# Kernel tuning notes

Hardware: AMD Instinct MI355X
Metric: run time of the kernel (lower is better)

The kernel has to match this reference:

```python
import jax, jax.numpy as jnp
import numpy as np

N = 50000   # nodes
E = 200000  # edges
C = 32      # conv_dim
ND = 75     # n_atom_features
ED = 12     # n_bond_features
L = 3       # num_layer
G = 500     # num graphs in batch
HID = 5     # neurons_message
EPS = 1e-5


def leaky(v):
    return jnp.where(v > 0, v, 0.01 * v)


def setup_inputs() -> dict:
    key = jax.random.key(0)
    ks = jax.random.split(key, 16)
    x = jax.random.normal(ks[0], (N, ND), jnp.float32)
    edge_index = jax.random.randint(ks[1], (2, E), 0, N, jnp.int32)
    edge_attr = jax.random.uniform(ks[2], (E, ED), jnp.float32)
    batch = jnp.sort(jax.random.randint(ks[3], (N,), 0, G, jnp.int32))
    return {
        "x": x,
        "edge_index": edge_index,
        "edge_attr": edge_attr,
        "batch": batch,
        "lin_W": jax.random.normal(ks[4], (ND, C), jnp.float32) * 0.1,
        "lin_b": jnp.zeros((C,), jnp.float32),
        "mes_W1": jax.random.normal(ks[5], (L, ED, HID), jnp.float32) * 0.3,
        "mes_b1": jnp.zeros((L, HID), jnp.float32),
        "mes_W2": jax.random.normal(ks[6], (L, HID, C * C), jnp.float32) * 0.05,
        "mes_b2": jnp.zeros((L, C * C), jnp.float32),
        "root_W": jax.random.normal(ks[7], (L, C, C), jnp.float32) * 0.1,
        "conv_b": jnp.zeros((L, C), jnp.float32),
        "bn_g": jnp.ones((L, C), jnp.float32),
        "bn_b": jnp.zeros((L, C), jnp.float32),
        "pred_W": jax.random.normal(ks[8], (C, 1), jnp.float32) * 0.1,
        "pred_b": jnp.zeros((1,), jnp.float32),
    }


def reference(x, edge_index, edge_attr, batch, lin_W, lin_b, mes_W1, mes_b1,
              mes_W2, mes_b2, root_W, conv_b, bn_g, bn_b, pred_W, pred_b):
    src, dst = edge_index[0], edge_index[1]
    # initial atom projection
    h = leaky(x @ lin_W + lin_b)  # [N, C]
    for l in range(L):
        # edge MLP -> per-edge weight matrix [E, C, C]
        w = jnp.maximum(edge_attr @ mes_W1[l] + mes_b1[l], 0.0)
        w = (w @ mes_W2[l] + mes_b2[l]).reshape(E, C, C)
        # gather source features, per-edge matmul, scatter-add to targets
        msg = jnp.einsum('ec,ecd->ed', h[src], w)  # [E, C]
        agg = jax.ops.segment_sum(msg, dst, num_segments=N)  # [N, C]
        out = agg + h @ root_W[l] + conv_b[l]
        # batch norm (batch statistics over nodes)
        mu = out.mean(axis=0)
        var = out.var(axis=0)
        out = (out - mu) / jnp.sqrt(var + EPS) * bn_g[l] + bn_b[l]
        if l < L - 1:
            out = leaky(out)
        h = out  # JK == 'last'
    # graph readout: scatter_add over batch ids, then prediction head
    g = jax.ops.segment_sum(h, batch, num_segments=G)  # [G, C]
    return g @ pred_W + pred_b  # [G, 1]
```

## Files before the change

### kernel.cpp

```cpp
#include <hip/hip_runtime.h>

namespace {

constexpr int kN = 50000, kE = 200000, kG = 500;
constexpr float kEps = 1e-5f;
constexpr int kNB = (kN + 255) / 256;
constexpr int kEB = (kE + 255) / 256;

typedef short v8s __attribute__((ext_vector_type(8)));
typedef float v4f __attribute__((ext_vector_type(4)));

__device__ __forceinline__ unsigned short bf16rn(float x) {
    unsigned u = __float_as_uint(x);
    return (unsigned short)((u + 0x7FFFu + ((u >> 16) & 1u)) >> 16);
}
__device__ __forceinline__ float bf16lo(unsigned p) { return __uint_as_float(p << 16); }
__device__ __forceinline__ float bf16hi(unsigned p) { return __uint_as_float(p & 0xFFFF0000u); }
__device__ __forceinline__ unsigned pk2(float a, float b) {
    return (unsigned)bf16rn(a) | ((unsigned)bf16rn(b) << 16);
}

__global__ __launch_bounds__(256) void zero_init(int* __restrict__ deg,
                                                 float* __restrict__ stats) {
    int i = blockIdx.x * 256 + threadIdx.x;
    if (i < kN) deg[i] = 0;
    if (i < 1536) stats[i] = 0.f;
}

__global__ __launch_bounds__(256) void deg_hist(
    const int* __restrict__ ei, int* __restrict__ deg)
{
    int e = blockIdx.x * 256 + threadIdx.x;
    if (e < kE) atomicAdd(&deg[ei[kE + e]], 1);
}

__global__ __launch_bounds__(1024) void init_h(
    const float* __restrict__ x, const float* __restrict__ W,
    const float* __restrict__ b, float* __restrict__ hbuf)
{
    __shared__ unsigned short sx[256 * 96];
    __shared__ unsigned short sW[32 * 96];
    int t = threadIdx.x;
    for (int i = t; i < 256 * 96; i += 1024) sx[i] = 0;
    for (int i = t; i < 32 * 96; i += 1024) sW[i] = 0;
    __syncthreads();
    int tb = blockIdx.x * 256;
    int cnt = min(256, kN - tb);
    for (int i = t; i < cnt * 75; i += 1024) {
        int n = i / 75, f = i - n * 75;
        sx[n * 96 + f] = bf16rn(x[(size_t)tb * 75 + i]);
    }
    for (int i = t; i < 75 * 32; i += 1024) {
        int f = i >> 5, c = i & 31;
        sW[c * 96 + f] = bf16rn(W[i]);
    }
    __syncthreads();
    int l15 = t & 15, quad = (t >> 4) & 3, w = t >> 6;
    #pragma unroll
    for (int tile = 0; tile < 2; ++tile) {
        v4f acc = {0.f, 0.f, 0.f, 0.f};
        #pragma unroll
        for (int kc = 0; kc < 3; ++kc) {
            v8s a  = *(const v8s*)&sx[(w * 16 + l15) * 96 + kc * 32 + quad * 8];
            v8s bb = *(const v8s*)&sW[(tile * 16 + l15) * 96 + kc * 32 + quad * 8];
            acc = __builtin_amdgcn_mfma_f32_16x16x32_bf16(a, bb, acc, 0, 0, 0);
        }
        int c = tile * 16 + l15;
        float bc = b[c];
        #pragma unroll
        for (int r = 0; r < 4; ++r) {
            int n = tb + w * 16 + quad * 4 + r;
            if (n < kN) {
                float v = acc[r] + bc;
                hbuf[(size_t)n * 32 + c] = v > 0.f ? v : 0.01f * v;
            }
        }
    }
}

__global__ __launch_bounds__(256) void scan_part(
    const int* __restrict__ deg, int* __restrict__ blkSum)
{
    __shared__ int sc[256];
    int t = threadIdx.x;
    int idx = blockIdx.x * 256 + t;
    sc[t] = (idx < kN) ? deg[idx] : 0;
    __syncthreads();
    #pragma unroll
    for (int off = 128; off > 0; off >>= 1) {
        if (t < off) sc[t] += sc[t + off];
        __syncthreads();
    }
    if (t == 0) blkSum[blockIdx.x] = sc[0];
}

__global__ __launch_bounds__(256) void scan_top(
    const int* __restrict__ blkSum, int* __restrict__ blkOff)
{
    __shared__ int sc[256];
    int t = threadIdx.x;
    int v = (t < kNB) ? blkSum[t] : 0;
    sc[t] = v;
    __syncthreads();
    #pragma unroll
    for (int off = 1; off < 256; off <<= 1) {
        int u = (t >= off) ? sc[t - off] : 0;
        __syncthreads();
        sc[t] += u;
        __syncthreads();
    }
    if (t < kNB) blkOff[t] = sc[t] - v;
}

__global__ __launch_bounds__(256) void scan_add(
    const int* __restrict__ deg, const int* __restrict__ blkOff,
    int* __restrict__ cursor)
{
    __shared__ int sc[256];
    int t = threadIdx.x;
    int idx = blockIdx.x * 256 + t;
    int v = (idx < kN) ? deg[idx] : 0;
    sc[t] = v;
    __syncthreads();
    #pragma unroll
    for (int off = 1; off < 256; off <<= 1) {
        int u = (t >= off) ? sc[t - off] : 0;
        __syncthreads();
        sc[t] += u;
        __syncthreads();
    }
    if (idx < kN) cursor[idx] = blkOff[blockIdx.x] + sc[t] - v;
}

__global__ __launch_bounds__(256) void hid_pre(
    const float* __restrict__ ea, const float* __restrict__ W1,
    const float* __restrict__ b1, const int* __restrict__ ei,
    int* __restrict__ cursor, uint4* __restrict__ hq)
{
    __shared__ float sE[256 * 13];
    __shared__ float sW[195];
    int t = threadIdx.x;
    for (int i = t; i < 195; i += 256) sW[i] = (i < 180) ? W1[i] : b1[i - 180];
    int base = blockIdx.x * 256;
    int cnt = min(256, kE - base);
    for (int i = t; i < cnt * 12; i += 256) {
        int el = i / 12, f = i - el * 12;
        sE[el * 13 + f] = ea[(size_t)base * 12 + i];
    }
    __syncthreads();
    if (t >= cnt) return;
    int e = base + t;
    unsigned src = (unsigned)ei[e];
    unsigned dst = (unsigned)ei[kE + e];
    int pos = atomicAdd(&cursor[dst], 1);
    float ef[12];
    #pragma unroll
    for (int j = 0; j < 12; ++j) ef[j] = sE[t * 13 + j];
    #pragma unroll
    for (int l = 0; l < 3; ++l) {
        float h[5];
        #pragma unroll
        for (int k = 0; k < 5; ++k) h[k] = sW[180 + l * 5 + k];
        #pragma unroll
        for (int f = 0; f < 12; ++f)
            #pragma unroll
            for (int k = 0; k < 5; ++k)
                h[k] = fmaf(ef[f], sW[l * 60 + f * 5 + k], h[k]);
        #pragma unroll
        for (int k = 0; k < 5; ++k) h[k] = h[k] > 0.f ? h[k] : 0.f;
        hq[(size_t)l * kE + pos] = make_uint4(
            pk2(h[0], h[1]), pk2(h[2], h[3]),
            (unsigned)bf16rn(h[4]) | (src << 16), dst);
    }
}

__global__ __launch_bounds__(1024) void y_root(
    const float* __restrict__ hbuf, float* __restrict__ obuf,
    const float* __restrict__ W2, const float* __restrict__ b2,
    const float* __restrict__ rW, const float* __restrict__ convb,
    const float* __restrict__ statsR,
    const float* __restrict__ gPrev, const float* __restrict__ bPrev,
    int first, unsigned* __restrict__ Ydw)
{
    __shared__ unsigned short sh[256 * 32];
    __shared__ unsigned short sB[256 * 32];
    int t = threadIdx.x;
    int tb = blockIdx.x * 256;
    int cnt = min(256, kN - tb);
    for (int i = t; i < 8192; i += 1024) {
        int co = i >> 5, c = i & 31, d = co >> 3, k = co & 7;
        float v = (k < 5) ? W2[k * 1024 + c * 32 + d]
                : (k == 5) ? b2[c * 32 + d]
                : (k == 6) ? rW[c * 32 + d] : 0.f;
        sB[co * 32 + c] = bf16rn(v);
    }
    if (first) {
        #pragma unroll
        for (int j = 0; j < 8; ++j) {
            int idx = t + j * 1024;
            int nl = idx >> 5, c = idx & 31;
            float v = (nl < cnt) ? hbuf[(size_t)(tb + nl) * 32 + c] : 0.f;
            sh[idx] = bf16rn(v);
        }
    } else {
        int c = t & 31;
        float sum = 0.f, sq = 0.f;
        #pragma unroll
        for (int r = 0; r < 8; ++r) {
            sum += statsR[r * 64 + c];
            sq  += statsR[r * 64 + 32 + c];
        }
        float mu = sum * (1.f / kN);
        float var = sq * (1.f / kN) - mu * mu;
        float ivg = rsqrtf(var + kEps) * gPrev[c];
        float bb = bPrev[c];
        #pragma unroll
        for (int j = 0; j < 8; ++j) {
            int idx = t + j * 1024;
            int nl = idx >> 5;
            float v = 0.f;
            if (nl < cnt) {
                float o = obuf[(size_t)(tb + nl) * 32 + c];
                v = (o - mu) * ivg + bb;
                v = v > 0.f ? v : 0.01f * v;
            }
            sh[idx] = bf16rn(v);
        }
    }
    __syncthreads();
    int l15 = t & 15, quad = (t >> 4) & 3, w = t >> 6;
    int n = tb + w * 16 + l15;
    v8s bn_ = *(const v8s*)&sh[(w * 16 + l15) * 32 + quad * 8];
    #pragma unroll
    for (int i = 0; i < 16; ++i) {
        v8s a = *(const v8s*)&sB[(i * 16 + l15) * 32 + quad * 8];
        v4f acc = {0.f, 0.f, 0.f, 0.f};
        acc = __builtin_amdgcn_mfma_f32_16x16x32_bf16(a, bn_, acc, 0, 0, 0);
        if (n < kN) {
            int cb = i * 16 + quad * 4;
            int d = cb >> 3, koff = cb & 7;
            if (koff == 0) {
                Ydw[(size_t)n * 96 + d * 3]     = pk2(acc[0], acc[1]);
                Ydw[(size_t)n * 96 + d * 3 + 1] = pk2(acc[2], acc[3]);
            } else {
                Ydw[(size_t)n * 96 + d * 3 + 2] = pk2(acc[0], acc[1]);
                obuf[(size_t)n * 32 + d] = acc[2] + convb[d];
            }
        }
    }
}

__global__ __launch_bounds__(256) void edge_scat(
    const uint4* __restrict__ hq, const unsigned* __restrict__ Ydw,
    float* __restrict__ obuf)
{
    int gid = blockIdx.x * 256 + threadIdx.x;
    int grp = gid >> 5;
    if (grp >= kE / 16) return;
    int d = gid & 31;
    int e0 = grp * 16;
    float acc = 0.f;
    unsigned cur = 0xFFFFFFFFu;
    #pragma unroll 4
    for (int i = 0; i < 16; ++i) {
        uint4 q = hq[e0 + i];
        unsigned src = q.z >> 16;
        const unsigned* yr = Ydw + (size_t)src * 96 + d * 3;
        unsigned p0 = yr[0], p1 = yr[1], p2 = yr[2];
        float m = bf16hi(p2);
        m = fmaf(bf16lo(q.x), bf16lo(p0), m);
        m = fmaf(bf16hi(q.x), bf16hi(p0), m);
        m = fmaf(bf16lo(q.y), bf16lo(p1), m);
        m = fmaf(bf16hi(q.y), bf16hi(p1), m);
        m = fmaf(bf16lo(q.z), bf16lo(p2), m);
        if (q.w != cur) {
            if (cur != 0xFFFFFFFFu) atomicAdd(&obuf[(size_t)cur * 32 + d], acc);
            cur = q.w; acc = m;
        } else acc += m;
    }
    if (cur != 0xFFFFFFFFu) atomicAdd(&obuf[(size_t)cur * 32 + d], acc);
}

__global__ __launch_bounds__(256) void bn_reduce(
    const float* __restrict__ obuf, float* __restrict__ statsR)
{
    __shared__ float ls[256];
    __shared__ float lq[256];
    int t = threadIdx.x;
    int c = t & 31, row = t >> 5;
    float s = 0.f, q = 0.f;
    for (int n = blockIdx.x * 8 + row; n < kN; n += gridDim.x * 8) {
        float v = obuf[(size_t)n * 32 + c];
        s += v; q += v * v;
    }
    ls[t] = s; lq[t] = q;
    __syncthreads();
    if (t < 128) { ls[t] += ls[t + 128]; lq[t] += lq[t + 128]; }
    __syncthreads();
    if (t < 64) { ls[t] += ls[t + 64]; lq[t] += lq[t + 64]; }
    __syncthreads();
    if (t < 32) {
        float* rep = statsR + (blockIdx.x & 7) * 64;
        atomicAdd(&rep[t], ls[t] + ls[t + 32]);
        atomicAdd(&rep[32 + t], lq[t] + lq[t + 32]);
    }
}

__global__ __launch_bounds__(256) void bn_norm_final(
    const float* __restrict__ obuf, const float* __restrict__ statsR,
    const float* __restrict__ g, const float* __restrict__ b,
    float* __restrict__ vbuf, const float* __restrict__ predW,
    float* __restrict__ out, const float* __restrict__ pred_b)
{
    int idx = blockIdx.x * 256 + threadIdx.x;
    if (idx < kG) out[idx] = pred_b[0];
    if (idx >= kN * 32) return;
    int c = idx & 31;
    float sum = 0.f, sq = 0.f;
    #pragma unroll
    for (int r = 0; r < 8; ++r) {
        sum += statsR[r * 64 + c];
        sq  += statsR[r * 64 + 32 + c];
    }
    float mu = sum * (1.f / kN);
    float var = sq * (1.f / kN) - mu * mu;
    float inv = rsqrtf(var + kEps);
    float v = (obuf[idx] - mu) * inv * g[c] + b[c];
    float pv = v * predW[c];
    #pragma unroll
    for (int off = 16; off > 0; off >>= 1) pv += __shfl_down(pv, off, 32);
    if (c == 0) vbuf[idx >> 5] = pv;
}

__global__ __launch_bounds__(256) void seg_readout(
    const float* __restrict__ vbuf, const int* __restrict__ batch,
    float* __restrict__ out)
{
    __shared__ float ls[kG];
    int t = threadIdx.x;
    for (int i = t; i < kG; i += 256) ls[i] = 0.f;
    __syncthreads();
    int base = blockIdx.x * 2048 + t * 8;
    int cur = -1; float acc = 0.f;
    #pragma unroll
    for (int i = 0; i < 8; ++i) {
        int n = base + i;
        if (n >= kN) break;
        int gi = batch[n];
        float val = vbuf[n];
        if (gi != cur) {
            if (cur >= 0) atomicAdd(&ls[cur], acc);
            cur = gi; acc = val;
        } else acc += val;
    }
    if (cur >= 0) atomicAdd(&ls[cur], acc);
    __syncthreads();
    for (int i = t; i < kG; i += 256) {
        float s = ls[i];
        if (s != 0.f) atomicAdd(&out[i], s);
    }
}

}

extern "C" void kernel_launch(void* const* d_in, const int* in_sizes, int n_in,
                              void* d_out, int out_size, void* d_ws, size_t ws_size,
                              hipStream_t stream)
{
    const float* x      = (const float*)d_in[0];
    const int*   ei     = (const int*)d_in[1];
    const float* ea     = (const float*)d_in[2];
    const int*   batch  = (const int*)d_in[3];
    const float* lin_W  = (const float*)d_in[4];
    const float* lin_b  = (const float*)d_in[5];
    const float* mes_W1 = (const float*)d_in[6];
    const float* mes_b1 = (const float*)d_in[7];
    const float* mes_W2 = (const float*)d_in[8];
    const float* mes_b2 = (const float*)d_in[9];
    const float* root_W = (const float*)d_in[10];
    const float* conv_b = (const float*)d_in[11];
    const float* bn_g   = (const float*)d_in[12];
    const float* bn_b   = (const float*)d_in[13];
    const float* pred_W = (const float*)d_in[14];
    const float* pred_b = (const float*)d_in[15];
    float* out = (float*)d_out;

    char* wsb = (char*)d_ws;
    float* stats = (float*)wsb;
    int* deg     = (int*)(wsb + 8192);
    int* cursor  = deg + kN;
    int* blkSum  = cursor + kN;
    int* blkOff  = blkSum + 256;
    float* hbuf  = (float*)(blkOff + 256);
    float* obuf  = hbuf + (size_t)kN * 32;
    unsigned short* Yus = (unsigned short*)(obuf + (size_t)kN * 32);
    unsigned* Ydw = (unsigned*)Yus;
    uint4* hq    = (uint4*)(Yus + (size_t)kN * 192);
    float* vbuf  = (float*)Yus;

    zero_init<<<kNB, 256, 0, stream>>>(deg, stats);
    deg_hist<<<kEB, 256, 0, stream>>>(ei, deg);
    init_h<<<kNB, 1024, 0, stream>>>(x, lin_W, lin_b, hbuf);
    scan_part<<<kNB, 256, 0, stream>>>(deg, blkSum);
    scan_top<<<1, 256, 0, stream>>>(blkSum, blkOff);
    scan_add<<<kNB, 256, 0, stream>>>(deg, blkOff, cursor);
    hid_pre<<<kEB, 256, 0, stream>>>(ea, mes_W1, mes_b1, ei, cursor, hq);

    int scatBlocks = ((kE / 16) * 32 + 255) / 256;
    for (int l = 0; l < 3; ++l) {
        y_root<<<kNB, 1024, 0, stream>>>(
            hbuf, obuf, mes_W2 + (size_t)l * 5120, mes_b2 + (size_t)l * 1024,
            root_W + (size_t)l * 1024, conv_b + l * 32,
            stats + (l ? (l - 1) * 512 : 0),
            bn_g + (l ? (l - 1) * 32 : 0), bn_b + (l ? (l - 1) * 32 : 0),
            l == 0 ? 1 : 0, Ydw);
        edge_scat<<<scatBlocks, 256, 0, stream>>>(
            hq + (size_t)l * kE, Ydw, obuf);
        bn_reduce<<<512, 256, 0, stream>>>(obuf, stats + l * 512);
    }

    bn_norm_final<<<(kN * 32 + 255) / 256, 256, 0, stream>>>(
        obuf, stats + 2 * 512, bn_g + 64, bn_b + 64, vbuf, pred_W, out, pred_b);
    seg_readout<<<(kN + 2047) / 2048, 256, 0, stream>>>(vbuf, batch, out);
}
```

Baseline: 290.1 us.

## Fold zero-init into init_h, merge scan kernels, shrink edge_scat groups to four edges

Zeroing of the degree and stats buffers moves into init_h, which removes one launch. The single-block scan_top is dropped: each scan_add block now sums the preceding block totals itself, which removes another launch and a serial dependency. edge_scat now gives each thread group 4 edges instead of 16, with all gathers issued up front. This raises parallelism and memory-level overlap but also increases the number of atomic adds to obuf.

Result: faster. 282.5 us (median of 2 runs) (-2.6%).

```diff
diff --git a/kernel.cpp b/kernel.cpp
--- a/kernel.cpp
+++ b/kernel.cpp
@@ -20,13 +20,6 @@
     return (unsigned)bf16rn(a) | ((unsigned)bf16rn(b) << 16);
 }
 
-__global__ __launch_bounds__(256) void zero_init(int* __restrict__ deg,
-                                                 float* __restrict__ stats) {
-    int i = blockIdx.x * 256 + threadIdx.x;
-    if (i < kN) deg[i] = 0;
-    if (i < 1536) stats[i] = 0.f;
-}
-
 __global__ __launch_bounds__(256) void deg_hist(
     const int* __restrict__ ei, int* __restrict__ deg)
 {
@@ -36,11 +29,17 @@
 
 __global__ __launch_bounds__(1024) void init_h(
     const float* __restrict__ x, const float* __restrict__ W,
-    const float* __restrict__ b, float* __restrict__ hbuf)
+    const float* __restrict__ b, float* __restrict__ hbuf,
+    int* __restrict__ deg, float* __restrict__ stats)
 {
     __shared__ unsigned short sx[256 * 96];
     __shared__ unsigned short sW[32 * 96];
     int t = threadIdx.x;
+    {
+        int z = blockIdx.x * 256 + t;
+        if (t < 256 && z < kN) deg[z] = 0;
+        if (blockIdx.x == 0) for (int i = t; i < 1536; i += 1024) stats[i] = 0.f;
+    }
     for (int i = t; i < 256 * 96; i += 1024) sx[i] = 0;
     for (int i = t; i < 32 * 96; i += 1024) sW[i] = 0;
     __syncthreads();
@@ -94,12 +93,24 @@
     if (t == 0) blkSum[blockIdx.x] = sc[0];
 }
 
-__global__ __launch_bounds__(256) void scan_top(
-    const int* __restrict__ blkSum, int* __restrict__ blkOff)
+__global__ __launch_bounds__(256) void scan_add(
+    const int* __restrict__ deg, const int* __restrict__ blkSum,
+    int* __restrict__ cursor)
 {
     __shared__ int sc[256];
-    int t = threadIdx.x;
-    int v = (t < kNB) ? blkSum[t] : 0;
+    __shared__ int sOff;
+    int t = threadIdx.x;
+    sc[t] = (t < blockIdx.x) ? blkSum[t] : 0;
+    __syncthreads();
+    #pragma unroll
+    for (int off = 128; off > 0; off >>= 1) {
+        if (t < off) sc[t] += sc[t + off];
+        __syncthreads();
+    }
+    if (t == 0) sOff = sc[0];
+    __syncthreads();
+    int idx = blockIdx.x * 256 + t;
+    int v = (idx < kN) ? deg[idx] : 0;
     sc[t] = v;
     __syncthreads();
     #pragma unroll
@@ -109,27 +120,7 @@
         sc[t] += u;
         __syncthreads();
     }
-    if (t < kNB) blkOff[t] = sc[t] - v;
-}
-
-__global__ __launch_bounds__(256) void scan_add(
-    const int* __restrict__ deg, const int* __restrict__ blkOff,
-    int* __restrict__ cursor)
-{
-    __shared__ int sc[256];
-    int t = threadIdx.x;
-    int idx = blockIdx.x * 256 + t;
-    int v = (idx < kN) ? deg[idx] : 0;
-    sc[t] = v;
-    __syncthreads();
-    #pragma unroll
-    for (int off = 1; off < 256; off <<= 1) {
-        int u = (t >= off) ? sc[t - off] : 0;
-        __syncthreads();
-        sc[t] += u;
-        __syncthreads();
-    }
-    if (idx < kN) cursor[idx] = blkOff[blockIdx.x] + sc[t] - v;
+    if (idx < kN) cursor[idx] = sOff + sc[t] - v;
 }
 
 __global__ __launch_bounds__(256) void hid_pre(
@@ -256,29 +247,50 @@
 {
     int gid = blockIdx.x * 256 + threadIdx.x;
     int grp = gid >> 5;
-    if (grp >= kE / 16) return;
     int d = gid & 31;
-    int e0 = grp * 16;
-    float acc = 0.f;
-    unsigned cur = 0xFFFFFFFFu;
-    #pragma unroll 4
-    for (int i = 0; i < 16; ++i) {
-        uint4 q = hq[e0 + i];
-        unsigned src = q.z >> 16;
-        const unsigned* yr = Ydw + (size_t)src * 96 + d * 3;
-        unsigned p0 = yr[0], p1 = yr[1], p2 = yr[2];
-        float m = bf16hi(p2);
-        m = fmaf(bf16lo(q.x), bf16lo(p0), m);
-        m = fmaf(bf16hi(q.x), bf16hi(p0), m);
-        m = fmaf(bf16lo(q.y), bf16lo(p1), m);
-        m = fmaf(bf16hi(q.y), bf16hi(p1), m);
-        m = fmaf(bf16lo(q.z), bf16lo(p2), m);
-        if (q.w != cur) {
-            if (cur != 0xFFFFFFFFu) atomicAdd(&obuf[(size_t)cur * 32 + d], acc);
-            cur = q.w; acc = m;
-        } else acc += m;
-    }
-    if (cur != 0xFFFFFFFFu) atomicAdd(&obuf[(size_t)cur * 32 + d], acc);
+    int e0 = grp * 4;
+    uint4 q0 = hq[e0], q1 = hq[e0 + 1], q2 = hq[e0 + 2], q3 = hq[e0 + 3];
+    const unsigned* y0 = Ydw + (size_t)(q0.z >> 16) * 96 + d * 3;
+    const unsigned* y1 = Ydw + (size_t)(q1.z >> 16) * 96 + d * 3;
+    const unsigned* y2 = Ydw + (size_t)(q2.z >> 16) * 96 + d * 3;
+    const unsigned* y3 = Ydw + (size_t)(q3.z >> 16) * 96 + d * 3;
+    unsigned p00 = y0[0], p01 = y0[1], p02 = y0[2];
+    unsigned p10 = y1[0], p11 = y1[1], p12 = y1[2];
+    unsigned p20 = y2[0], p21 = y2[1], p22 = y2[2];
+    unsigned p30 = y3[0], p31 = y3[1], p32 = y3[2];
+    float m0 = bf16hi(p02);
+    m0 = fmaf(bf16lo(q0.x), bf16lo(p00), m0);
+    m0 = fmaf(bf16hi(q0.x), bf16hi(p00), m0);
+    m0 = fmaf(bf16lo(q0.y), bf16lo(p01), m0);
+    m0 = fmaf(bf16hi(q0.y), bf16hi(p01), m0);
+    m0 = fmaf(bf16lo(q0.z), bf16lo(p02), m0);
+    float m1 = bf16hi(p12);
+    m1 = fmaf(bf16lo(q1.x), bf16lo(p10), m1);
+    m1 = fmaf(bf16hi(q1.x), bf16hi(p10), m1);
+    m1 = fmaf(bf16lo(q1.y), bf16lo(p11), m1);
+    m1 = fmaf(bf16hi(q1.y), bf16hi(p11), m1);
+    m1 = fmaf(bf16lo(q1.z), bf16lo(p12), m1);
+    float m2 = bf16hi(p22);
+    m2 = fmaf(bf16lo(q2.x), bf16lo(p20), m2);
+    m2 = fmaf(bf16hi(q2.x), bf16hi(p20), m2);
+    m2 = fmaf(bf16lo(q2.y), bf16lo(p21), m2);
+    m2 = fmaf(bf16hi(q2.y), bf16hi(p21), m2);
+    m2 = fmaf(bf16lo(q2.z), bf16lo(p22), m2);
+    float m3 = bf16hi(p32);
+    m3 = fmaf(bf16lo(q3.x), bf16lo(p30), m3);
+    m3 = fmaf(bf16hi(q3.x), bf16hi(p30), m3);
+    m3 = fmaf(bf16lo(q3.y), bf16lo(p31), m3);
+    m3 = fmaf(bf16hi(q3.y), bf16hi(p31), m3);
+    m3 = fmaf(bf16lo(q3.z), bf16lo(p32), m3);
+    float acc = m0;
+    unsigned cur = q0.w;
+    if (q1.w == cur) acc += m1;
+    else { atomicAdd(&obuf[(size_t)cur * 32 + d], acc); cur = q1.w; acc = m1; }
+    if (q2.w == cur) acc += m2;
+    else { atomicAdd(&obuf[(size_t)cur * 32 + d], acc); cur = q2.w; acc = m2; }
+    if (q3.w == cur) acc += m3;
+    else { atomicAdd(&obuf[(size_t)cur * 32 + d], acc); cur = q3.w; acc = m3; }
+    atomicAdd(&obuf[(size_t)cur * 32 + d], acc);
 }
 
 __global__ __launch_bounds__(256) void bn_reduce(
@@ -390,23 +402,20 @@
     int* deg     = (int*)(wsb + 8192);
     int* cursor  = deg + kN;
     int* blkSum  = cursor + kN;
-    int* blkOff  = blkSum + 256;
-    float* hbuf  = (float*)(blkOff + 256);
+    float* hbuf  = (float*)(blkSum + 256);
     float* obuf  = hbuf + (size_t)kN * 32;
     unsigned short* Yus = (unsigned short*)(obuf + (size_t)kN * 32);
     unsigned* Ydw = (unsigned*)Yus;
     uint4* hq    = (uint4*)(Yus + (size_t)kN * 192);
     float* vbuf  = (float*)Yus;
 
-    zero_init<<<kNB, 256, 0, stream>>>(deg, stats);
+    init_h<<<kNB, 1024, 0, stream>>>(x, lin_W, lin_b, hbuf, deg, stats);
     deg_hist<<<kEB, 256, 0, stream>>>(ei, deg);
-    init_h<<<kNB, 1024, 0, stream>>>(x, lin_W, lin_b, hbuf);
     scan_part<<<kNB, 256, 0, stream>>>(deg, blkSum);
-    scan_top<<<1, 256, 0, stream>>>(blkSum, blkOff);
-    scan_add<<<kNB, 256, 0, stream>>>(deg, blkOff, cursor);
+    scan_add<<<kNB, 256, 0, stream>>>(deg, blkSum, cursor);
     hid_pre<<<kEB, 256, 0, stream>>>(ea, mes_W1, mes_b1, ei, cursor, hq);
 
-    int scatBlocks = ((kE / 16) * 32 + 255) / 256;
+    int scatBlocks = (kE / 4) * 32 / 256;
     for (int l = 0; l < 3; ++l) {
         y_root<<<kNB, 1024, 0, stream>>>(
             hbuf, obuf, mes_W2 + (size_t)l * 5120, mes_b2 + (size_t)l * 1024,
```
